# Optimization experiments

Measured on AMD Instinct MI355X. Metric: run time of the kernel, lower is better.

## Reference

```python
import jax, jax.numpy as jnp
import numpy as np
import math

B, S, D, H, F = 2, 2048, 1024, 16, 4096
HD = D // H
EPS = 1e-5

def _alibi_slopes(n_heads):
    # n_heads is a power of 2 here (16): m_i = start * start**i, start = 2^(-2^(-(log2(n)-3)))
    start = 2.0 ** (-(2.0 ** (-(math.log2(n_heads) - 3))))
    return np.array([start * (start ** i) for i in range(n_heads)], dtype=np.float32)

SLOPES = jnp.asarray(_alibi_slopes(H))  # (H,)


def setup_inputs() -> dict:
    key = jax.random.key(0)
    ks = jax.random.split(key, 8)
    s = 0.02
    return {
        "x":  jax.random.normal(ks[0], (B, S, D), jnp.float32),
        "Wq": jax.random.normal(ks[1], (D, D), jnp.float32) * s,
        "Wk": jax.random.normal(ks[2], (D, D), jnp.float32) * s,
        "Wv": jax.random.normal(ks[3], (D, D), jnp.float32) * s,
        "Wo": jax.random.normal(ks[4], (D, D), jnp.float32) * s,
        "bo": jnp.zeros((D,), jnp.float32),
        "W1": jax.random.normal(ks[5], (F, D), jnp.float32) * s,
        "b1": jnp.zeros((F,), jnp.float32),
        "W2": jax.random.normal(ks[6], (D, F), jnp.float32) * s,
        "b2": jnp.zeros((D,), jnp.float32),
        "g1": jnp.ones((D,), jnp.float32),
        "be1": jnp.zeros((D,), jnp.float32),
        "g2": jnp.ones((D,), jnp.float32),
        "be2": jnp.zeros((D,), jnp.float32),
    }


def _layernorm(h, g, b):
    mu = jnp.mean(h, axis=-1, keepdims=True)
    var = jnp.mean((h - mu) ** 2, axis=-1, keepdims=True)
    return (h - mu) * jax.lax.rsqrt(var + EPS) * g + b


def reference(x, Wq, Wk, Wv, Wo, bo, W1, b1, W2, b2, g1, be1, g2, be2):
    # --- pre-norm ALiBi attention ---
    h = _layernorm(x, g1, be1)
    q = (h @ Wq.T).reshape(B, S, H, HD).transpose(0, 2, 1, 3)  # (B,H,S,HD)
    k = (h @ Wk.T).reshape(B, S, H, HD).transpose(0, 2, 1, 3)
    v = (h @ Wv.T).reshape(B, S, H, HD).transpose(0, 2, 1, 3)
    scores = jnp.einsum("bhqd,bhkd->bhqk", q, k) / math.sqrt(HD)
    pos = jnp.arange(S)
    dist = (pos[None, :] - pos[:, None]).astype(jnp.float32)      # (S,S): j - i
    bias = SLOPES[:, None, None] * dist[None, :, :]               # (H,S,S)
    attn = jax.nn.softmax(scores + bias[None], axis=-1)
    ao = jnp.einsum("bhqk,bhkd->bhqd", attn, v)
    ao = ao.transpose(0, 2, 1, 3).reshape(B, S, D) @ Wo.T + bo
    x = x + ao
    # --- pre-norm FFN ---
    h2 = _layernorm(x, g2, be2)
    ff = jax.nn.relu(h2 @ W1.T + b1) @ W2.T + b2
    return x + ff
```

## Files before the change

### kernel.cpp

```cpp
#include <hip/hip_runtime.h>
#include <hip/hip_bf16.h>
#include <stdint.h>

typedef unsigned short u16;
typedef __attribute__((ext_vector_type(8))) short short8;
typedef __attribute__((ext_vector_type(4))) float f32x4;

#define S_LEN 2048
#define D_DIM 1024
#define NHEAD 16
#define HDIM 64
#define NROWS 4096

__device__ __forceinline__ u16 f2bf(float f) {
  union { float f; uint32_t u; } c; c.f = f;
  uint32_t r = (c.u + 0x7fffu + ((c.u >> 16) & 1u)) >> 16;
  return (u16)r;
}

__device__ __forceinline__ uint32_t pack_bf2(float a, float b) {
  __hip_bfloat162 h = __float22bfloat162_rn(float2{a, b});
  union { __hip_bfloat162 h; uint32_t u; } c; c.h = h;
  return c.u;
}

__device__ __forceinline__ void gload_lds16(const void* g, void* l) {
  typedef const __attribute__((address_space(1))) unsigned int gq_t;
  typedef __attribute__((address_space(3))) unsigned int lq_t;
  __builtin_amdgcn_global_load_lds((gq_t*)(uintptr_t)g,
                                   (lq_t*)(uint32_t)(uintptr_t)l, 16, 0, 0);
}

__global__ __launch_bounds__(256) void cast_all(const float* __restrict__ Wq,
                                                const float* __restrict__ Wk,
                                                const float* __restrict__ Wv,
                                                const float* __restrict__ Wo,
                                                const float* __restrict__ W1,
                                                const float* __restrict__ W2,
                                                u16* __restrict__ wqkv,
                                                u16* __restrict__ wo,
                                                u16* __restrict__ w1,
                                                u16* __restrict__ w2) {
  int i = blockIdx.x * 256 + threadIdx.x;
  const float* src;
  u16* dst;
  int rel;
  if (i < 786432) {
    int ws = i / 262144;
    rel = i - ws * 262144;
    src = (ws == 0) ? Wq : ((ws == 1) ? Wk : Wv);
    dst = wqkv + (size_t)ws * 1048576;
  } else if (i < 1048576) {
    rel = i - 786432; src = Wo; dst = wo;
  } else if (i < 2097152) {
    rel = i - 1048576; src = W1; dst = w1;
  } else {
    rel = i - 2097152; src = W2; dst = w2;
  }
  float4 v = ((const float4*)src)[rel];
  ((ushort4*)dst)[rel] = make_ushort4(f2bf(v.x), f2bf(v.y), f2bf(v.z), f2bf(v.w));
}

__global__ __launch_bounds__(256) void ln_kernel(const float* __restrict__ x,
                                                 const float* __restrict__ g,
                                                 const float* __restrict__ be,
                                                 u16* __restrict__ out) {
  int row = blockIdx.x;
  int tid = threadIdx.x;
  const float4 v = ((const float4*)(x + (size_t)row * D_DIM))[tid];
  float s = v.x + v.y + v.z + v.w;
  float s2 = v.x * v.x + v.y * v.y + v.z * v.z + v.w * v.w;
#pragma unroll
  for (int off = 1; off < 64; off <<= 1) {
    s += __shfl_xor(s, off);
    s2 += __shfl_xor(s2, off);
  }
  __shared__ float ss[4], ss2[4];
  if ((tid & 63) == 0) { ss[tid >> 6] = s; ss2[tid >> 6] = s2; }
  __syncthreads();
  s = ss[0] + ss[1] + ss[2] + ss[3];
  s2 = ss2[0] + ss2[1] + ss2[2] + ss2[3];
  float mu = s * (1.0f / D_DIM);
  float var = s2 * (1.0f / D_DIM) - mu * mu;
  float rs = rsqrtf(var + 1e-5f);
  float4 gv = ((const float4*)g)[tid];
  float4 bv = ((const float4*)be)[tid];
  ushort4 o = make_ushort4(f2bf((v.x - mu) * rs * gv.x + bv.x),
                           f2bf((v.y - mu) * rs * gv.y + bv.y),
                           f2bf((v.z - mu) * rs * gv.z + bv.z),
                           f2bf((v.w - mu) * rs * gv.w + bv.w));
  ((ushort4*)(out + (size_t)row * D_DIM))[tid] = o;
}

template <int EPI>
__global__ __launch_bounds__(512, 2) void gemm_bt2(const u16* __restrict__ A,
                                                   const u16* __restrict__ Bw,
                                                   void* __restrict__ Cout,
                                                   const float* __restrict__ bias,
                                                   int M, int N, int K) {
  __shared__ u16 lsA[2][256 * 32];
  __shared__ u16 lsB[2][256 * 32];
  const int tid = threadIdx.x;
  const int wid = tid >> 6, lane = tid & 63;
  const int l4 = lane & 15, lh = lane >> 4;
  const int wr = wid >> 2, wc = wid & 3;
  const int nbn = N >> 8;
  const int nwg = (M >> 8) * nbn;
  const int t0 = (blockIdx.x & 7) * (nwg >> 3) + (blockIdx.x >> 3);
  const int bm = t0 / nbn, bn = t0 % nbn;

  f32x4 acc[8][4];
#pragma unroll
  for (int i = 0; i < 8; ++i)
#pragma unroll
    for (int j = 0; j < 4; ++j) acc[i][j] = (f32x4){0.f, 0.f, 0.f, 0.f};

  const int srow = lane >> 2;
  const int sblk = (lane & 3) ^ ((lane >> 3) & 3);
  const u16* Abase = A + ((size_t)bm * 256 + wid * 32 + srow) * K + sblk * 8;
  const u16* Bbase = Bw + ((size_t)bn * 256 + wid * 32 + srow) * K + sblk * 8;
  const size_t r16 = (size_t)16 * K;
#define STAGE(BUF, KT)                                              \
  {                                                                 \
    int ko = (KT) * 32;                                             \
    gload_lds16(Abase + ko, (char*)lsA[BUF] + wid * 2048);          \
    gload_lds16(Abase + r16 + ko, (char*)lsA[BUF] + wid * 2048 + 1024); \
    gload_lds16(Bbase + ko, (char*)lsB[BUF] + wid * 2048);          \
    gload_lds16(Bbase + r16 + ko, (char*)lsB[BUF] + wid * 2048 + 1024); \
  }

  const int swz = (lh ^ ((l4 >> 1) & 3)) << 4;
  int aoff[8], boff[4];
#pragma unroll
  for (int m = 0; m < 8; ++m) aoff[m] = (wr * 128 + m * 16 + l4) * 64 + swz;
#pragma unroll
  for (int n = 0; n < 4; ++n) boff[n] = (wc * 64 + n * 16 + l4) * 64 + swz;

  STAGE(0, 0);
  __syncthreads();
  int cur = 0;
  const int NT = K >> 5;

  for (int t = 0; t < NT; ++t) {
    if (t + 1 < NT) STAGE(cur ^ 1, t + 1);
    const char* La = (const char*)lsA[cur];
    const char* Lb = (const char*)lsB[cur];
    short8 aF[4], bF[4], aG[4];
#pragma unroll
    for (int m = 0; m < 4; ++m) aF[m] = *(const short8*)(La + aoff[m]);
#pragma unroll
    for (int n = 0; n < 4; ++n) bF[n] = *(const short8*)(Lb + boff[n]);
    __builtin_amdgcn_s_setprio(1);
#pragma unroll
    for (int m = 0; m < 4; ++m)
#pragma unroll
      for (int n = 0; n < 4; ++n)
        acc[m][n] = __builtin_amdgcn_mfma_f32_16x16x32_bf16(aF[m], bF[n], acc[m][n], 0, 0, 0);
    __builtin_amdgcn_s_setprio(0);
#pragma unroll
    for (int m = 0; m < 4; ++m) aG[m] = *(const short8*)(La + aoff[m + 4]);
    __builtin_amdgcn_s_setprio(1);
#pragma unroll
    for (int m = 0; m < 4; ++m)
#pragma unroll
      for (int n = 0; n < 4; ++n)
        acc[m + 4][n] = __builtin_amdgcn_mfma_f32_16x16x32_bf16(aG[m], bF[n], acc[m + 4][n], 0, 0, 0);
    __builtin_amdgcn_s_setprio(0);
    if (t + 1 < NT) __syncthreads();
    cur ^= 1;
  }

  const int row0 = bm * 256 + wr * 128 + lh * 4;
  const int col0 = bn * 256 + wc * 64 + l4;
#pragma unroll
  for (int m = 0; m < 8; ++m) {
#pragma unroll
    for (int n = 0; n < 4; ++n) {
      int col = col0 + n * 16;
#pragma unroll
      for (int r = 0; r < 4; ++r) {
        size_t idx = (size_t)(row0 + m * 16 + r) * N + col;
        float v = acc[m][n][r];
        if (EPI == 0) {
          ((u16*)Cout)[idx] = f2bf(v);
        } else {
          v += bias[col];
          ((u16*)Cout)[idx] = f2bf(v > 0.f ? v : 0.f);
        }
      }
    }
  }
#undef STAGE
}

template <int EPI>
__global__ __launch_bounds__(512, 2) void gemm_bt3(const u16* __restrict__ A,
                                                   const u16* __restrict__ Bw,
                                                   void* __restrict__ Cout,
                                                   const float* __restrict__ bias,
                                                   const float* __restrict__ resid,
                                                   int M, int N, int K, int ksl) {
  __shared__ u16 lsA[2][256 * 32];
  __shared__ u16 lsB[2][128 * 32];
  const int tid = threadIdx.x;
  const int wid = tid >> 6, lane = tid & 63;
  const int l4 = lane & 15, lh = lane >> 4;
  const int wr = wid >> 1, wc = wid & 1;
  const int nbn = N >> 7;
  const int nwgs = (M >> 8) * nbn;
  const int slice = blockIdx.x / nwgs;
  const int id0 = blockIdx.x % nwgs;
  const int t0 = (id0 & 7) * (nwgs >> 3) + (id0 >> 3);
  const int bm = t0 / nbn, bn = t0 % nbn;
  const int Ks = K / ksl;

  f32x4 acc[4][4];
#pragma unroll
  for (int i = 0; i < 4; ++i)
#pragma unroll
    for (int j = 0; j < 4; ++j) acc[i][j] = (f32x4){0.f, 0.f, 0.f, 0.f};

  const int srow = lane >> 2;
  const int sblk = (lane & 3) ^ ((lane >> 3) & 3);
  const u16* Abase = A + ((size_t)bm * 256 + wid * 16 + srow) * K + (size_t)slice * Ks + sblk * 8;
  const u16* Bbase = Bw + ((size_t)bn * 128 + wid * 16 + srow) * K + (size_t)slice * Ks + sblk * 8;
  const size_t r128 = (size_t)128 * K;
#define STAGE(BUF, KT)                                               \
  {                                                                  \
    int ko = (KT) * 32;                                              \
    gload_lds16(Abase + ko, (char*)lsA[BUF] + wid * 1024);           \
    gload_lds16(Abase + r128 + ko, (char*)lsA[BUF] + 8192 + wid * 1024); \
    gload_lds16(Bbase + ko, (char*)lsB[BUF] + wid * 1024);           \
  }

  const int swz = (lh ^ ((l4 >> 1) & 3)) << 4;
  int aoff[4], boff[4];
#pragma unroll
  for (int m = 0; m < 4; ++m) aoff[m] = (wr * 64 + m * 16 + l4) * 64 + swz;
#pragma unroll
  for (int n = 0; n < 4; ++n) boff[n] = (wc * 64 + n * 16 + l4) * 64 + swz;

  STAGE(0, 0);
  __syncthreads();
  int cur = 0;
  const int NT = Ks >> 5;

  for (int t = 0; t < NT; ++t) {
    if (t + 1 < NT) STAGE(cur ^ 1, t + 1);
    const char* La = (const char*)lsA[cur];
    const char* Lb = (const char*)lsB[cur];
    short8 aF[4], bF[4];
#pragma unroll
    for (int m = 0; m < 4; ++m) aF[m] = *(const short8*)(La + aoff[m]);
#pragma unroll
    for (int n = 0; n < 4; ++n) bF[n] = *(const short8*)(Lb + boff[n]);
    __builtin_amdgcn_s_setprio(1);
#pragma unroll
    for (int m = 0; m < 4; ++m)
#pragma unroll
      for (int n = 0; n < 4; ++n)
        acc[m][n] = __builtin_amdgcn_mfma_f32_16x16x32_bf16(aF[m], bF[n], acc[m][n], 0, 0, 0);
    __builtin_amdgcn_s_setprio(0);
    if (t + 1 < NT) __syncthreads();
    cur ^= 1;
  }

  const int row0 = bm * 256 + wr * 64 + lh * 4;
  const int col0 = bn * 128 + wc * 64 + l4;
  float* Cp = (float*)Cout + (size_t)slice * M * N;
#pragma unroll
  for (int m = 0; m < 4; ++m) {
#pragma unroll
    for (int n = 0; n < 4; ++n) {
      int col = col0 + n * 16;
#pragma unroll
      for (int r = 0; r < 4; ++r) {
        size_t idx = (size_t)(row0 + m * 16 + r) * N + col;
        float v = acc[m][n][r];
        if (EPI == 1) {
          ((float*)Cout)[idx] = v + bias[col] + resid[idx];
        } else {
          Cp[idx] = v;
        }
      }
    }
  }
#undef STAGE
}

template <int EPI>
__global__ __launch_bounds__(256) void gemm_bt(const u16* __restrict__ A,
                                               const u16* __restrict__ Bw,
                                               void* __restrict__ Cout,
                                               const float* __restrict__ bias,
                                               const float* __restrict__ resid,
                                               int M, int N, int K, int ksl) {
  __shared__ u16 lsA[128 * 64];
  __shared__ u16 lsB[128 * 64];
  const int tid = threadIdx.x;
  const int wid = tid >> 6, lane = tid & 63;
  const int l4 = lane & 15, lh = lane >> 4;
  const int nbn = N >> 7;
  const int nwgs = (M >> 7) * nbn;
  const int slice = blockIdx.x / nwgs;
  const int id0 = blockIdx.x % nwgs;
  const int t = (id0 & 7) * (nwgs >> 3) + (id0 >> 3);
  const int bm = t / nbn, bn = t % nbn;
  const int wr = wid >> 1, wc = wid & 1;
  const int Ks = K / ksl;

  f32x4 acc[4][4];
#pragma unroll
  for (int i = 0; i < 4; ++i)
#pragma unroll
    for (int j = 0; j < 4; ++j) acc[i][j] = (f32x4){0.f, 0.f, 0.f, 0.f};

  const u16* Ab = A + (size_t)bm * 128 * K + (size_t)slice * Ks;
  const u16* Bb = Bw + (size_t)bn * 128 * K + (size_t)slice * Ks;
  const int srow = (lane >> 3);
  const int scol = (lane & 7) * 8;

  for (int k0 = 0; k0 < Ks; k0 += 64) {
#pragma unroll
    for (int c = 0; c < 4; ++c) {
      int ch = wid * 4 + c;
      int row = ch * 8 + srow;
      gload_lds16(Ab + (size_t)row * K + k0 + scol, &lsA[ch * 512]);
      gload_lds16(Bb + (size_t)row * K + k0 + scol, &lsB[ch * 512]);
    }
    __syncthreads();
#pragma unroll
    for (int ks = 0; ks < 2; ++ks) {
      short8 af[4], bf[4];
#pragma unroll
      for (int i = 0; i < 4; ++i) {
        af[i] = *(const short8*)&lsA[(wr * 64 + i * 16 + l4) * 64 + ks * 32 + lh * 8];
        bf[i] = *(const short8*)&lsB[(wc * 64 + i * 16 + l4) * 64 + ks * 32 + lh * 8];
      }
#pragma unroll
      for (int i = 0; i < 4; ++i)
#pragma unroll
        for (int j = 0; j < 4; ++j)
          acc[i][j] = __builtin_amdgcn_mfma_f32_16x16x32_bf16(af[i], bf[j], acc[i][j], 0, 0, 0);
    }
    __syncthreads();
  }

  const int row0 = bm * 128 + wr * 64;
  const int col0 = bn * 128 + wc * 64;
  float* Cp = (float*)Cout + (size_t)slice * M * N;
#pragma unroll
  for (int i = 0; i < 4; ++i) {
#pragma unroll
    for (int j = 0; j < 4; ++j) {
      int col = col0 + j * 16 + l4;
#pragma unroll
      for (int r = 0; r < 4; ++r) {
        int row = row0 + i * 16 + lh * 4 + r;
        size_t idx = (size_t)row * N + col;
        float v = acc[i][j][r];
        if (EPI == 1) {
          ((float*)Cout)[idx] = v + bias[col] + resid[idx];
        } else {
          Cp[idx] = v;
        }
      }
    }
  }
}

__global__ __launch_bounds__(256) void reduce2_kernel(const float* __restrict__ p0,
                                                      const float* __restrict__ p1,
                                                      const float* __restrict__ resid,
                                                      const float* __restrict__ bias,
                                                      float* __restrict__ out) {
  for (int i = blockIdx.x * 256 + threadIdx.x; i < (NROWS * D_DIM) / 4;
       i += gridDim.x * 256) {
    float4 a = ((const float4*)p0)[i];
    float4 b = ((const float4*)p1)[i];
    float4 r = ((const float4*)resid)[i];
    float4 bb = ((const float4*)bias)[i & 255];
    float4 o;
    o.x = a.x + b.x + r.x + bb.x;
    o.y = a.y + b.y + r.y + bb.y;
    o.z = a.z + b.z + r.z + bb.z;
    o.w = a.w + b.w + r.w + bb.w;
    ((float4*)out)[i] = o;
  }
}

__global__ __launch_bounds__(256) void transpose_v(const u16* __restrict__ qkv,
                                                   u16* __restrict__ vt) {
  const int gw = blockIdx.x * 4 + (threadIdx.x >> 6);
  const int lane = threadIdx.x & 63;
  const int bh = gw >> 5;
  const int st = gw & 31;
  const int b = bh >> 4, h = bh & 15;
  const u16* src = qkv + (size_t)(b * S_LEN + st * 64) * 3072 + 2048 + h * 64 + lane;
  short8 acc8[8];
#pragma unroll
  for (int o = 0; o < 8; ++o)
#pragma unroll
    for (int i = 0; i < 8; ++i)
      acc8[o][i] = (short)src[(size_t)(o * 8 + i) * 3072];
  u16* dst = vt + ((size_t)bh * 64 + lane) * S_LEN + st * 64;
#pragma unroll
  for (int o = 0; o < 8; ++o) *(short8*)(dst + o * 8) = acc8[o];
}

__global__ __launch_bounds__(256, 4) void attn_kernel(const u16* __restrict__ qkv,
                                                      const u16* __restrict__ vt,
                                                      u16* __restrict__ ao,
                                                      float* __restrict__ pO,
                                                      float* __restrict__ pML) {
  const int id = blockIdx.x;
  const int sub = id & 63;
  const int ugrp = id >> 6;
  int h, j;
  if (ugrp < 15) { h = 15 - ugrp / 3; j = ugrp % 3; }
  else if (ugrp < 19) { h = 10 - ((ugrp - 15) >> 1); j = (ugrp - 15) & 1; }
  else { h = 27 - ugrp; j = 0; }
  const int b = sub >> 5, qt = sub & 31;
  const int bh = b * 16 + h;
  const int tid = threadIdx.x;
  const int wid = tid >> 6, lane = tid & 63;
  const int l4 = lane & 15, lh = lane >> 4;

  __shared__ u16 Kt[2][64 * 64];
  __shared__ u16 Vt[2][64 * 64];
  __shared__ u16 Pt[4][16 * 64];

  const size_t RS = 3 * D_DIM;
  const u16* base = qkv + (size_t)b * S_LEN * RS + h * HDIM;
  const u16* kbase = base + D_DIM;
  const u16* vtb = vt + (size_t)bh * HDIM * S_LEN;
  char* PtW = (char*)Pt[wid];

  short8 qf[2];
  {
    const u16* qp = base + (size_t)(qt * 64 + wid * 16 + l4) * RS + lh * 8;
    qf[0] = *(const short8*)qp;
    qf[1] = *(const short8*)(qp + 32);
  }

  int koff[4][2];
#pragma unroll
  for (int nb = 0; nb < 4; ++nb)
#pragma unroll
    for (int ks = 0; ks < 2; ++ks) {
      int row = nb * 16 + l4;
      koff[nb][ks] = row * 128 + (((ks * 32 + lh * 8) * 2) ^ ((row & 7) << 4));
    }
  int poff[2];
#pragma unroll
  for (int ks = 0; ks < 2; ++ks)
    poff[ks] = l4 * 128 + (((ks * 64 + lh * 16)) ^ ((l4 & 7) << 4));
  int pwoff[4];
#pragma unroll
  for (int nb = 0; nb < 4; ++nb)
    pwoff[nb] = l4 * 128 + (((lh * 8 + nb * 32)) ^ ((l4 & 7) << 4));

  const float slope2 = exp2f(-0.5f * (float)(h + 1)) * 1.44269504088896f;
  const float scale2 = 0.125f * 1.44269504088896f;
  const int ibase = lh * 4 - (qt * 64 + wid * 16 + l4);
  float bc[4][4];
#pragma unroll
  for (int nb = 0; nb < 4; ++nb)
#pragma unroll
    for (int r = 0; r < 4; ++r)
      bc[nb][r] = slope2 * (float)(ibase + 16 * nb + r);

  int nt = (int)ceilf(40.0f / (64.0f * slope2)) + 1;
  if (nt > 32) nt = 32;
  const int nsp = (nt + 11) / 12;
  const int ktmin = 32 - nt;
  const int hi = 31 - j * 12;
  int lo = hi - 11;
  if (lo < ktmin) lo = ktmin;

  float m = -1e30f;
  f32x4 lacc = (f32x4){0.f, 0.f, 0.f, 0.f};
  f32x4 accO[4];
#pragma unroll
  for (int nd = 0; nd < 4; ++nd) accO[nd] = (f32x4){0.f, 0.f, 0.f, 0.f};
  const short8 vones = {(short)0x3F80, (short)0x3F80, (short)0x3F80, (short)0x3F80,
                        (short)0x3F80, (short)0x3F80, (short)0x3F80, (short)0x3F80};

  const int srow = tid >> 3;
  const int sc8 = (tid & 7) * 8;
  const int swo = srow * 128 + ((sc8 * 2) ^ ((srow & 7) << 4));
  short8 kreg[2], vreg[2];
#define STAGE_LOAD(KT)                                                              \
  {                                                                                 \
    kreg[0] = *(const short8*)(kbase + (size_t)((KT)*64 + srow) * RS + sc8);        \
    kreg[1] = *(const short8*)(kbase + (size_t)((KT)*64 + srow + 32) * RS + sc8);   \
    vreg[0] = *(const short8*)(vtb + (size_t)srow * S_LEN + (KT)*64 + sc8);         \
    vreg[1] = *(const short8*)(vtb + (size_t)(srow + 32) * S_LEN + (KT)*64 + sc8);  \
  }
#define STAGE_WRITE(B)                                   \
  {                                                      \
    *(short8*)((char*)Kt[B] + swo) = kreg[0];            \
    *(short8*)((char*)Kt[B] + swo + 4096) = kreg[1];     \
    *(short8*)((char*)Vt[B] + swo) = vreg[0];            \
    *(short8*)((char*)Vt[B] + swo + 4096) = vreg[1];     \
  }

  STAGE_LOAD(hi);
  STAGE_WRITE(0);
  __syncthreads();
  int cur = 0;
  float ktoff = slope2 * 64.0f * (float)hi;
  const float dko = slope2 * 64.0f;

  for (int kt = hi; kt >= lo; --kt) {
    if (kt > lo) STAGE_LOAD(kt - 1);
    const char* Kc = (const char*)Kt[cur];
    const char* Vc = (const char*)Vt[cur];

    f32x4 sacc[4];
#pragma unroll
    for (int nb = 0; nb < 4; ++nb) sacc[nb] = (f32x4){0.f, 0.f, 0.f, 0.f};
    __builtin_amdgcn_s_setprio(1);
#pragma unroll
    for (int ks = 0; ks < 2; ++ks)
#pragma unroll
      for (int nb = 0; nb < 4; ++nb) {
        short8 kf = *(const short8*)(Kc + koff[nb][ks]);
        sacc[nb] = __builtin_amdgcn_mfma_f32_16x16x32_bf16(kf, qf[ks], sacc[nb], 0, 0, 0);
      }
    __builtin_amdgcn_s_setprio(0);

    float p[4][4];
#pragma unroll
    for (int nb = 0; nb < 4; ++nb)
#pragma unroll
      for (int r = 0; r < 4; ++r)
        p[nb][r] = fmaf(sacc[nb][r], scale2, bc[nb][r]);

    float mx0 = fmaxf(fmaxf(p[0][0], p[0][1]), fmaxf(p[0][2], p[0][3]));
    float mx1 = fmaxf(fmaxf(p[1][0], p[1][1]), fmaxf(p[1][2], p[1][3]));
    float mx2 = fmaxf(fmaxf(p[2][0], p[2][1]), fmaxf(p[2][2], p[2][3]));
    float mx3 = fmaxf(fmaxf(p[3][0], p[3][1]), fmaxf(p[3][2], p[3][3]));
    float tm = fmaxf(fmaxf(mx0, mx1), fmaxf(mx2, mx3));
    tm = fmaxf(tm, __shfl_xor(tm, 16));
    tm = fmaxf(tm, __shfl_xor(tm, 32));

    float mm = m - ktoff;
    if (__any(tm > mm)) {
      float mn = fmaxf(mm, tm);
      float corr = exp2f(mm - mn);
      m = mn + ktoff;
      mm = mn;
      float cb[4];
#pragma unroll
      for (int r = 0; r < 4; ++r)
        cb[r] = __shfl(corr, (lane & 48) | (lh * 4 + r));
#pragma unroll
      for (int nd = 0; nd < 4; ++nd)
#pragma unroll
        for (int r = 0; r < 4; ++r) accO[nd][r] *= cb[r];
#pragma unroll
      for (int r = 0; r < 4; ++r) lacc[r] *= cb[r];
    }

#pragma unroll
    for (int nb = 0; nb < 4; ++nb)
#pragma unroll
      for (int r = 0; r < 4; ++r) p[nb][r] = exp2f(p[nb][r] - mm);

#pragma unroll
    for (int nb = 0; nb < 4; ++nb) {
      uint32_t w0 = pack_bf2(p[nb][0], p[nb][1]);
      uint32_t w1 = pack_bf2(p[nb][2], p[nb][3]);
      *(uint2*)(PtW + pwoff[nb]) = make_uint2(w0, w1);
    }
    asm volatile("s_waitcnt lgkmcnt(0)" ::: "memory");

    __builtin_amdgcn_s_setprio(1);
#pragma unroll
    for (int ks = 0; ks < 2; ++ks) {
      short8 pf = *(const short8*)(PtW + poff[ks]);
      lacc = __builtin_amdgcn_mfma_f32_16x16x32_bf16(pf, vones, lacc, 0, 0, 0);
#pragma unroll
      for (int nd = 0; nd < 4; ++nd) {
        short8 vf = *(const short8*)(Vc + koff[nd][ks]);
        accO[nd] = __builtin_amdgcn_mfma_f32_16x16x32_bf16(pf, vf, accO[nd], 0, 0, 0);
      }
    }
    __builtin_amdgcn_s_setprio(0);

    if (kt > lo) STAGE_WRITE(cur ^ 1);
    __syncthreads();
    cur ^= 1;
    ktoff -= dko;
  }

  if (nsp == 1) {
    float ib[4];
#pragma unroll
    for (int r = 0; r < 4; ++r) ib[r] = 1.0f / lacc[r];
    u16* aop = ao + ((size_t)(b * S_LEN + qt * 64 + wid * 16 + lh * 4)) * D_DIM + h * HDIM;
#pragma unroll
    for (int nd = 0; nd < 4; ++nd)
#pragma unroll
      for (int r = 0; r < 4; ++r)
        aop[(size_t)r * D_DIM + nd * 16 + l4] = f2bf(accO[nd][r] * ib[r]);
  } else {
    const int sbase = (h <= 10) ? (h - 9) * 2 : 4 + (h - 11) * 3;
    const int pidx = sub * 19 + sbase + j;
    float* Op = pO + (size_t)pidx * 4096;
#pragma unroll
    for (int nd = 0; nd < 4; ++nd)
#pragma unroll
      for (int r = 0; r < 4; ++r)
        Op[(wid * 16 + lh * 4 + r) * 64 + nd * 16 + l4] = accO[nd][r];
    float mq[4];
#pragma unroll
    for (int r = 0; r < 4; ++r)
      mq[r] = __shfl(m, (lane & 48) | (lh * 4 + r));
    if (l4 == 0) {
      float* mlp = pML + (size_t)pidx * 128 + (wid * 16 + lh * 4) * 2;
#pragma unroll
      for (int r = 0; r < 4; ++r) {
        mlp[r * 2] = mq[r];
        mlp[r * 2 + 1] = lacc[r];
      }
    }
  }
#undef STAGE_LOAD
#undef STAGE_WRITE
}

__global__ __launch_bounds__(256) void attn_combine(const float* __restrict__ pO,
                                                    const float* __restrict__ pML,
                                                    u16* __restrict__ ao) {
  const int g = blockIdx.x;
  const int sub = g & 63;
  const int h = 9 + (g >> 6);
  const int b = sub >> 5, qt = sub & 31;
  const int nsp = (h <= 10) ? 2 : 3;
  const int sbase = (h <= 10) ? (h - 9) * 2 : 4 + (h - 11) * 3;
  const int pidx0 = sub * 19 + sbase;
  const int tid = threadIdx.x;
  const int row = tid >> 2;
  const int d0 = (tid & 3) * 16;

  float mj[3], lj[3];
#pragma unroll
  for (int k = 0; k < 3; ++k) { mj[k] = -1e30f; lj[k] = 0.f; }
  for (int k = 0; k < nsp; ++k) {
    mj[k] = pML[(size_t)(pidx0 + k) * 128 + row * 2];
    lj[k] = pML[(size_t)(pidx0 + k) * 128 + row * 2 + 1];
  }
  float ms = fmaxf(mj[0], fmaxf(mj[1], mj[2]));
  float w[3];
  float lsum = 0.f;
#pragma unroll
  for (int k = 0; k < 3; ++k) {
    w[k] = exp2f(mj[k] - ms);
    lsum += w[k] * lj[k];
  }
  float inv = 1.0f / lsum;

  u16* aop = ao + ((size_t)(b * S_LEN + qt * 64 + row)) * D_DIM + h * HDIM + d0;
#pragma unroll
  for (int c = 0; c < 4; ++c) {
    float4 o = {0.f, 0.f, 0.f, 0.f};
    for (int k = 0; k < nsp; ++k) {
      const float4 v = *(const float4*)(pO + (size_t)(pidx0 + k) * 4096 + row * 64 + d0 + c * 4);
      o.x += w[k] * v.x; o.y += w[k] * v.y; o.z += w[k] * v.z; o.w += w[k] * v.w;
    }
    ushort4 u4 = make_ushort4(f2bf(o.x * inv), f2bf(o.y * inv), f2bf(o.z * inv), f2bf(o.w * inv));
    *(ushort4*)(aop + c * 4) = u4;
  }
}

extern "C" void kernel_launch(void* const* d_in, const int* in_sizes, int n_in,
                              void* d_out, int out_size, void* d_ws, size_t ws_size,
                              hipStream_t stream) {
  const float* x   = (const float*)d_in[0];
  const float* Wq  = (const float*)d_in[1];
  const float* Wk  = (const float*)d_in[2];
  const float* Wv  = (const float*)d_in[3];
  const float* Wo  = (const float*)d_in[4];
  const float* bo  = (const float*)d_in[5];
  const float* W1  = (const float*)d_in[6];
  const float* b1  = (const float*)d_in[7];
  const float* W2  = (const float*)d_in[8];
  const float* b2  = (const float*)d_in[9];
  const float* g1  = (const float*)d_in[10];
  const float* be1 = (const float*)d_in[11];
  const float* g2  = (const float*)d_in[12];
  const float* be2 = (const float*)d_in[13];

  char* p = (char*)d_ws;
  u16* wqkv = (u16*)p; p += (size_t)3072 * 1024 * 2;
  u16* wo   = (u16*)p; p += (size_t)1024 * 1024 * 2;
  u16* w1   = (u16*)p; p += (size_t)4096 * 1024 * 2;
  u16* w2   = (u16*)p; p += (size_t)4096 * 1024 * 2;
  u16* hb   = (u16*)p; p += (size_t)4096 * 1024 * 2;
  u16* qkvb = (u16*)p; p += (size_t)4096 * 3072 * 2;
  u16* aob  = (u16*)p; p += (size_t)4096 * 1024 * 2;
  float* x1 = (float*)p; p += (size_t)4096 * 1024 * 4;
  u16* h2b  = (u16*)p; p += (size_t)4096 * 1024 * 2;
  u16* ff1  = (u16*)p; p += (size_t)4096 * 4096 * 2;
  u16* vt   = ff1;
  float* pO = (float*)(ff1 + (size_t)4 * 1024 * 1024);
  float* pML = pO + (size_t)1216 * 4096;
  float* pk = (float*)hb;

  cast_all<<<12288, 256, 0, stream>>>(Wq, Wk, Wv, Wo, W1, W2, wqkv, wo, w1, w2);

  ln_kernel<<<4096, 256, 0, stream>>>(x, g1, be1, hb);
  gemm_bt2<0><<<16 * 12, 512, 0, stream>>>(hb, wqkv, qkvb, nullptr, 4096, 3072, 1024);
  transpose_v<<<256, 256, 0, stream>>>(qkvb, vt);
  attn_kernel<<<1792, 256, 0, stream>>>(qkvb, vt, aob, pO, pML);
  attn_combine<<<448, 256, 0, stream>>>(pO, pML, aob);
  gemm_bt<1><<<32 * 8, 256, 0, stream>>>(aob, wo, x1, bo, x, 4096, 1024, 1024, 1);
  ln_kernel<<<4096, 256, 0, stream>>>(x1, g2, be2, h2b);
  gemm_bt2<2><<<16 * 16, 512, 0, stream>>>(h2b, w1, ff1, b1, 4096, 4096, 1024);
  gemm_bt3<3><<<2 * 16 * 8, 512, 0, stream>>>(ff1, w2, pk, nullptr, nullptr, 4096, 1024, 4096, 2);
  reduce2_kernel<<<2048, 256, 0, stream>>>(pk, pk + (size_t)4096 * 1024, x1, b2, (float*)d_out);
}
```

Measured before the change: 234.7 us.

## Use 512-row tiles with 4-way split-K and bf16 partials for FFN down-projection

Replaces the W2 GEMM with a variant that uses 512x128 output tiles, with each wave computing 128 rows in two MFMA phases. It splits K four ways instead of two and stores the partial sums as bf16 instead of fp32. The reduce kernel now sums four bf16 partials and adds bias and residual. The goal is to raise per-block reuse of the B operand and keep the grid at 256 blocks while halving partial-sum traffic per slice. The cost is more LDS and registers per block, plus added rounding error from bf16 partials.

```diff
diff --git a/kernel.cpp b/kernel.cpp
--- a/kernel.cpp
+++ b/kernel.cpp
@@ -16,6 +16,11 @@
   union { float f; uint32_t u; } c; c.f = f;
   uint32_t r = (c.u + 0x7fffu + ((c.u >> 16) & 1u)) >> 16;
   return (u16)r;
+}
+
+__device__ __forceinline__ float bf2f(u16 v) {
+  union { uint32_t u; float f; } c; c.u = ((uint32_t)v) << 16;
+  return c.f;
 }
 
 __device__ __forceinline__ uint32_t pack_bf2(float a, float b) {
@@ -193,50 +198,49 @@
 #undef STAGE
 }
 
-template <int EPI>
-__global__ __launch_bounds__(512, 2) void gemm_bt3(const u16* __restrict__ A,
+__global__ __launch_bounds__(512, 2) void gemm_bt4(const u16* __restrict__ A,
                                                    const u16* __restrict__ Bw,
-                                                   void* __restrict__ Cout,
-                                                   const float* __restrict__ bias,
-                                                   const float* __restrict__ resid,
+                                                   u16* __restrict__ Cpk,
                                                    int M, int N, int K, int ksl) {
-  __shared__ u16 lsA[2][256 * 32];
+  __shared__ u16 lsA[2][512 * 32];
   __shared__ u16 lsB[2][128 * 32];
   const int tid = threadIdx.x;
   const int wid = tid >> 6, lane = tid & 63;
   const int l4 = lane & 15, lh = lane >> 4;
   const int wr = wid >> 1, wc = wid & 1;
   const int nbn = N >> 7;
-  const int nwgs = (M >> 8) * nbn;
+  const int nwgs = (M >> 9) * nbn;
   const int slice = blockIdx.x / nwgs;
   const int id0 = blockIdx.x % nwgs;
   const int t0 = (id0 & 7) * (nwgs >> 3) + (id0 >> 3);
   const int bm = t0 / nbn, bn = t0 % nbn;
   const int Ks = K / ksl;
 
-  f32x4 acc[4][4];
-#pragma unroll
-  for (int i = 0; i < 4; ++i)
+  f32x4 acc[8][4];
+#pragma unroll
+  for (int i = 0; i < 8; ++i)
 #pragma unroll
     for (int j = 0; j < 4; ++j) acc[i][j] = (f32x4){0.f, 0.f, 0.f, 0.f};
 
   const int srow = lane >> 2;
   const int sblk = (lane & 3) ^ ((lane >> 3) & 3);
-  const u16* Abase = A + ((size_t)bm * 256 + wid * 16 + srow) * K + (size_t)slice * Ks + sblk * 8;
+  const u16* Abase = A + ((size_t)bm * 512 + wid * 64 + srow) * K + (size_t)slice * Ks + sblk * 8;
   const u16* Bbase = Bw + ((size_t)bn * 128 + wid * 16 + srow) * K + (size_t)slice * Ks + sblk * 8;
-  const size_t r128 = (size_t)128 * K;
-#define STAGE(BUF, KT)                                               \
-  {                                                                  \
-    int ko = (KT) * 32;                                              \
-    gload_lds16(Abase + ko, (char*)lsA[BUF] + wid * 1024);           \
-    gload_lds16(Abase + r128 + ko, (char*)lsA[BUF] + 8192 + wid * 1024); \
-    gload_lds16(Bbase + ko, (char*)lsB[BUF] + wid * 1024);           \
+  const size_t r16 = (size_t)16 * K;
+#define STAGE(BUF, KT)                                                   \
+  {                                                                      \
+    int ko = (KT) * 32;                                                  \
+    gload_lds16(Abase + ko, (char*)lsA[BUF] + wid * 4096);               \
+    gload_lds16(Abase + r16 + ko, (char*)lsA[BUF] + wid * 4096 + 1024);  \
+    gload_lds16(Abase + 2 * r16 + ko, (char*)lsA[BUF] + wid * 4096 + 2048); \
+    gload_lds16(Abase + 3 * r16 + ko, (char*)lsA[BUF] + wid * 4096 + 3072); \
+    gload_lds16(Bbase + ko, (char*)lsB[BUF] + wid * 1024);               \
   }
 
   const int swz = (lh ^ ((l4 >> 1) & 3)) << 4;
-  int aoff[4], boff[4];
-#pragma unroll
-  for (int m = 0; m < 4; ++m) aoff[m] = (wr * 64 + m * 16 + l4) * 64 + swz;
+  int aoff[8], boff[4];
+#pragma unroll
+  for (int m = 0; m < 8; ++m) aoff[m] = (wr * 128 + m * 16 + l4) * 64 + swz;
 #pragma unroll
   for (int n = 0; n < 4; ++n) boff[n] = (wc * 64 + n * 16 + l4) * 64 + swz;
 
@@ -249,7 +253,7 @@
     if (t + 1 < NT) STAGE(cur ^ 1, t + 1);
     const char* La = (const char*)lsA[cur];
     const char* Lb = (const char*)lsB[cur];
-    short8 aF[4], bF[4];
+    short8 aF[4], bF[4], aG[4];
 #pragma unroll
     for (int m = 0; m < 4; ++m) aF[m] = *(const short8*)(La + aoff[m]);
 #pragma unroll
@@ -261,27 +265,31 @@
       for (int n = 0; n < 4; ++n)
         acc[m][n] = __builtin_amdgcn_mfma_f32_16x16x32_bf16(aF[m], bF[n], acc[m][n], 0, 0, 0);
     __builtin_amdgcn_s_setprio(0);
+#pragma unroll
+    for (int m = 0; m < 4; ++m) aG[m] = *(const short8*)(La + aoff[m + 4]);
+    __builtin_amdgcn_s_setprio(1);
+#pragma unroll
+    for (int m = 0; m < 4; ++m)
+#pragma unroll
+      for (int n = 0; n < 4; ++n)
+        acc[m + 4][n] = __builtin_amdgcn_mfma_f32_16x16x32_bf16(aG[m], bF[n], acc[m + 4][n], 0, 0, 0);
+    __builtin_amdgcn_s_setprio(0);
     if (t + 1 < NT) __syncthreads();
     cur ^= 1;
   }
 
-  const int row0 = bm * 256 + wr * 64 + lh * 4;
+  const int row0 = bm * 512 + wr * 128 + lh * 4;
   const int col0 = bn * 128 + wc * 64 + l4;
-  float* Cp = (float*)Cout + (size_t)slice * M * N;
-#pragma unroll
-  for (int m = 0; m < 4; ++m) {
+  u16* Cp = Cpk + (size_t)slice * M * N;
+#pragma unroll
+  for (int m = 0; m < 8; ++m) {
 #pragma unroll
     for (int n = 0; n < 4; ++n) {
       int col = col0 + n * 16;
 #pragma unroll
       for (int r = 0; r < 4; ++r) {
         size_t idx = (size_t)(row0 + m * 16 + r) * N + col;
-        float v = acc[m][n][r];
-        if (EPI == 1) {
-          ((float*)Cout)[idx] = v + bias[col] + resid[idx];
-        } else {
-          Cp[idx] = v;
-        }
+        Cp[idx] = f2bf(acc[m][n][r]);
       }
     }
   }
@@ -369,24 +377,29 @@
   }
 }
 
-__global__ __launch_bounds__(256) void reduce2_kernel(const float* __restrict__ p0,
-                                                      const float* __restrict__ p1,
+__global__ __launch_bounds__(256) void reduce4_kernel(const u16* __restrict__ pk,
                                                       const float* __restrict__ resid,
                                                       const float* __restrict__ bias,
                                                       float* __restrict__ out) {
-  for (int i = blockIdx.x * 256 + threadIdx.x; i < (NROWS * D_DIM) / 4;
-       i += gridDim.x * 256) {
-    float4 a = ((const float4*)p0)[i];
-    float4 b = ((const float4*)p1)[i];
-    float4 r = ((const float4*)resid)[i];
-    float4 bb = ((const float4*)bias)[i & 255];
-    float4 o;
-    o.x = a.x + b.x + r.x + bb.x;
-    o.y = a.y + b.y + r.y + bb.y;
-    o.z = a.z + b.z + r.z + bb.z;
-    o.w = a.w + b.w + r.w + bb.w;
-    ((float4*)out)[i] = o;
-  }
+  const size_t SL = (size_t)NROWS * D_DIM;
+  int i = blockIdx.x * 256 + threadIdx.x;
+  short8 p0 = *(const short8*)(pk + (size_t)i * 8);
+  short8 p1 = *(const short8*)(pk + SL + (size_t)i * 8);
+  short8 p2 = *(const short8*)(pk + 2 * SL + (size_t)i * 8);
+  short8 p3 = *(const short8*)(pk + 3 * SL + (size_t)i * 8);
+  int col = (i * 8) & (D_DIM - 1);
+  float4 b0 = *(const float4*)(bias + col);
+  float4 b1 = *(const float4*)(bias + col + 4);
+  float4 r0 = ((const float4*)resid)[i * 2];
+  float4 r1 = ((const float4*)resid)[i * 2 + 1];
+  float o[8];
+#pragma unroll
+  for (int j = 0; j < 8; ++j)
+    o[j] = bf2f((u16)p0[j]) + bf2f((u16)p1[j]) + bf2f((u16)p2[j]) + bf2f((u16)p3[j]);
+  float4 w0 = {o[0] + b0.x + r0.x, o[1] + b0.y + r0.y, o[2] + b0.z + r0.z, o[3] + b0.w + r0.w};
+  float4 w1 = {o[4] + b1.x + r1.x, o[5] + b1.y + r1.y, o[6] + b1.z + r1.z, o[7] + b1.w + r1.w};
+  ((float4*)out)[i * 2] = w0;
+  ((float4*)out)[i * 2 + 1] = w1;
 }
 
 __global__ __launch_bounds__(256) void transpose_v(const u16* __restrict__ qkv,
@@ -707,7 +720,7 @@
   u16* vt   = ff1;
   float* pO = (float*)(ff1 + (size_t)4 * 1024 * 1024);
   float* pML = pO + (size_t)1216 * 4096;
-  float* pk = (float*)hb;
+  u16* pk = hb;
 
   cast_all<<<12288, 256, 0, stream>>>(Wq, Wk, Wv, Wo, W1, W2, wqkv, wo, w1, w2);
 
@@ -719,6 +732,6 @@
   gemm_bt<1><<<32 * 8, 256, 0, stream>>>(aob, wo, x1, bo, x, 4096, 1024, 1024, 1);
   ln_kernel<<<4096, 256, 0, stream>>>(x1, g2, be2, h2b);
   gemm_bt2<2><<<16 * 16, 512, 0, stream>>>(h2b, w1, ff1, b1, 4096, 4096, 1024);
-  gemm_bt3<3><<<2 * 16 * 8, 512, 0, stream>>>(ff1, w2, pk, nullptr, nullptr, 4096, 1024, 4096, 2);
-  reduce2_kernel<<<2048, 256, 0, stream>>>(pk, pk + (size_t)4096 * 1024, x1, b2, (float*)d_out);
-}
+  gemm_bt4<<<4 * 8 * 8, 512, 0, stream>>>(ff1, w2, pk, 4096, 1024, 4096, 4);
+  reduce4_kernel<<<2048, 256, 0, stream>>>(pk, x1, b2, (float*)d_out);
+}
```

New measurement: 229.9 us. 2.0% less time.
